# Optimization experiments

Hardware: AMD Instinct MI355X
Metric: run time of the kernel (lower is better)

Reference implementation:

```python
import jax, jax.numpy as jnp
import numpy as np

N_HEADS = 2
WINDOW = 4
BLOCK = 256


def _get_rel_emb(emb, length):
    # emb: [1, 2*WINDOW+1, K] -> [1, 2*length-1, K]
    pad = max(length - (WINDOW + 1), 0)
    start = max((WINDOW + 1) - length, 0)
    e = jnp.pad(emb, ((0, 0), (pad, pad), (0, 0)))
    return e[:, start:start + 2 * length - 1]


def _rel_to_abs(x):
    # x: [b, h, l, 2l-1] -> [b, h, l, l] (skew trick)
    b, h, l, _ = x.shape
    x = jnp.pad(x, ((0, 0), (0, 0), (0, 0), (0, 1))).reshape(b, h, 2 * l * l)
    x = jnp.pad(x, ((0, 0), (0, 0), (0, l - 1))).reshape(b, h, l + 1, 2 * l - 1)
    return x[:, :, :l, l - 1:]


def _abs_to_rel(x):
    # x: [b, h, l, l] -> [b, h, l, 2l-1] (inverse skew)
    b, h, l, _ = x.shape
    x = jnp.pad(x, ((0, 0), (0, 0), (0, 0), (0, l - 1))).reshape(b, h, l * (2 * l - 1))
    x = jnp.pad(x, ((0, 0), (0, 0), (l, 0))).reshape(b, h, l, 2 * l)
    return x[:, :, :, 1:]


def _attention(x, c, attn_mask, Wq, bq, Wk, bk, Wv, bv, Wo, bo, emb_rel_k, emb_rel_v):
    B, C, T = x.shape
    H, K = N_HEADS, C // N_HEADS
    # projections (torch Linear on [B,T,C])
    q = (jnp.einsum('bct,cd->btd', x, Wq) + bq).reshape(B, T, H, K).transpose(0, 2, 1, 3)
    k = (jnp.einsum('bct,cd->btd', c, Wk) + bk).reshape(B, T, H, K).transpose(0, 2, 1, 3)
    v = (jnp.einsum('bct,cd->btd', c, Wv) + bv).reshape(B, T, H, K).transpose(0, 2, 1, 3)
    qs = q / jnp.sqrt(jnp.float32(K))
    scores = jnp.einsum('bhtk,bhsk->bhts', qs, k)  # [B,H,T,T]
    # relative-position key logits (heads_share=True -> single table)
    rel_k = _get_rel_emb(emb_rel_k, T)[0]          # [2T-1, K]
    rel_logits = jnp.einsum('bhtk,rk->bhtr', qs, rel_k)
    scores = scores + _rel_to_abs(rel_logits)
    # proximal bias: -log1p(|i-j|)
    r = jnp.arange(T, dtype=jnp.float32)
    scores = scores - jnp.log1p(jnp.abs(r[:, None] - r[None, :]))[None, None]
    # attn mask + block-local mask (block mask active because mask is given)
    ij = jnp.arange(T)
    block_ok = jnp.abs(ij[:, None] - ij[None, :]) <= BLOCK
    valid = (attn_mask != 0) & block_ok[None, None]
    scores = jnp.where(valid, scores, jnp.float32(-1e4))
    p = jax.nn.softmax(scores, axis=-1)
    out = jnp.einsum('bhts,bhsk->bhtk', p, v)
    # relative-position value contribution
    rel_v = _get_rel_emb(emb_rel_v, T)[0]          # [2T-1, K]
    out = out + jnp.einsum('bhtr,rk->bhtk', _abs_to_rel(p), rel_v)
    out = out.transpose(0, 2, 1, 3).reshape(B, T, C)
    y = jnp.einsum('btd,do->bto', out, Wo) + bo
    return y.transpose(0, 2, 1)  # [B, out_channels, T]


def setup_inputs() -> dict:
    key = jax.random.key(0)
    ks = jax.random.split(key, 8)
    B, C, T = 4, 192, 2048
    K = C // N_HEADS
    s = jnp.float32(0.05)
    rel_std = jnp.float32(K ** -0.5)
    return {
        'x': jax.random.normal(ks[0], (B, C, T), jnp.float32),
        'c': jax.random.normal(ks[1], (B, C, T), jnp.float32),
        'Wq': jax.random.normal(ks[2], (C, C), jnp.float32) * s,
        'bq': jnp.zeros((C,), jnp.float32),
        'Wk': jax.random.normal(ks[3], (C, C), jnp.float32) * s,
        'bk': jnp.zeros((C,), jnp.float32),
        'Wv': jax.random.normal(ks[4], (C, C), jnp.float32) * s,
        'bv': jnp.zeros((C,), jnp.float32),
        'Wo': jax.random.normal(ks[5], (C, C), jnp.float32) * s,
        'bo': jnp.zeros((C,), jnp.float32),
        'emb_rel_k': jax.random.normal(ks[6], (1, 2 * WINDOW + 1, K), jnp.float32) * rel_std,
        'emb_rel_v': jax.random.normal(ks[7], (1, 2 * WINDOW + 1, K), jnp.float32) * rel_std,
        'attn_mask': jnp.ones((B, 1, T, T), jnp.int32),
    }


def reference(x, c, Wq, bq, Wk, bk, Wv, bv, Wo, bo, emb_rel_k, emb_rel_v, attn_mask):
    return _attention(x, c, attn_mask, Wq, bq, Wk, bk, Wv, bv, Wo, bo, emb_rel_k, emb_rel_v)
```

## Files before the change

kernel.cpp:

```cpp
#include <hip/hip_runtime.h>
#include <hip/hip_bf16.h>

#define B_DIM 4
#define C_DIM 192
#define T_SEQ 2048
#define H_DIM 2
#define K_DIM 96
#define BAND 256
#define IT 16
#define WSLOT 544
#define W_P 548
#define PMW 17

typedef __attribute__((ext_vector_type(8))) short bf16x8;
typedef __attribute__((ext_vector_type(4))) short bf16x4;
typedef __attribute__((ext_vector_type(4))) float f32x4;
#define MFMA16 __builtin_amdgcn_mfma_f32_16x16x32_bf16

__device__ __forceinline__ float bfbits2f(short s) {
    union { short s; __hip_bfloat16 h; } u; u.s = s; return __bfloat162float(u.h);
}
__device__ __forceinline__ short f2bf_bits(float f) {
    union { __hip_bfloat16 h; short s; } u; u.h = __float2bfloat16(f); return u.s;
}

#define OFF_WT(m)  ((size_t)(m)*73728)
#define OFF_BQS    ((size_t)294912)
#define OFF_RELKBF ((size_t)295680)
#define OFF_LT     ((size_t)298752)
#define OFF_PM     ((size_t)299840)
#define OFF_QBF    ((size_t)856896)
#define OFF_KBF    (OFF_QBF + 3145728)
#define OFF_VTB    (OFF_KBF + 3145728)
#define OFF_OBTC   (OFF_VTB + 3145728)

__global__ __launch_bounds__(256)
void prep_kernel(const float* __restrict__ Wq, const float* __restrict__ Wk,
                 const float* __restrict__ Wv, const float* __restrict__ Wo,
                 const float* __restrict__ bq, const float* __restrict__ relk,
                 const int* __restrict__ mask, char* __restrict__ ws)
{
    const float qscale = 0.10206207261596577f;
    const int bidx = blockIdx.x;
    const int tid  = threadIdx.x;

    if (bidx < 576) {
        const size_t idx = (size_t)bidx*256 + tid;
        const int mi  = (int)(idx / 36864);
        const int rem = (int)(idx % 36864);
        const int c = rem / C_DIM, d = rem % C_DIM;
        const float* src = (mi == 0) ? Wq : (mi == 1) ? Wk : (mi == 2) ? Wv : Wo;
        float v = src[c*C_DIM + d];
        if (mi == 0) v *= qscale;
        ((short*)(ws + OFF_WT(mi)))[d*C_DIM + c] = f2bf_bits(v);
        return;
    }
    if (bidx < 1120) {
        const int idx = (bidx - 576)*256 + tid;
        const int b = idx / (T_SEQ*PMW);
        const int rem = idx % (T_SEQ*PMW);
        const int i = rem / PMW, w = rem % PMW;
        const int jlo = max(0, (i & ~15) - BAND);
        const int* mrow = mask + ((size_t)b*T_SEQ + i)*T_SEQ;
        unsigned bits = 0;
        #pragma unroll
        for (int g4 = 0; g4 < 8; ++g4) {
            const int jg = jlo + 32*w + 4*g4;
            if (jg + 3 < T_SEQ) {
                const int4 mv = *reinterpret_cast<const int4*>(mrow + jg);
                bits |= (unsigned)(mv.x != 0) << (4*g4);
                bits |= (unsigned)(mv.y != 0) << (4*g4+1);
                bits |= (unsigned)(mv.z != 0) << (4*g4+2);
                bits |= (unsigned)(mv.w != 0) << (4*g4+3);
            } else {
                #pragma unroll
                for (int e = 0; e < 4; ++e)
                    if (jg + e < T_SEQ && mrow[jg+e] != 0) bits |= 1u << (4*g4+e);
            }
        }
        ((unsigned*)(ws + OFF_PM))[idx] = bits;
        return;
    }
    if (tid < C_DIM)
        ((float*)(ws + OFF_BQS))[tid] = bq[tid]*qscale;
    short* rkb = (short*)(ws + OFF_RELKBF);
    for (int idx = tid; idx < 16*K_DIM; idx += 256) {
        const int row = idx / K_DIM;
        rkb[idx] = (row < 9) ? f2bf_bits(relk[idx]) : (short)0;
    }
    float* ltws = (float*)(ws + OFF_LT);
    for (int idx = tid; idx < 257; idx += 256) ltws[idx] = log1pf((float)idx);
}

__global__ __launch_bounds__(256)
void proj_kernel(const float* __restrict__ x, const float* __restrict__ cin,
                 const float* __restrict__ bk, const float* __restrict__ bv,
                 char* __restrict__ ws)
{
    __shared__ short xs[IT*C_DIM];
    __shared__ short cs[IT*C_DIM];
    const int b    = blockIdx.x >> 8;
    const int half = (blockIdx.x >> 7) & 1;
    const int t0   = (blockIdx.x & 127) * IT;
    const int tid  = threadIdx.x;
    const int wave = tid >> 6, lane = tid & 63;
    const int q4 = lane >> 4, lr = lane & 15;

    for (int l = tid; l < 768; l += 256) {
        const int cr = l >> 2, u = l & 3;
        const size_t off = (size_t)(b*C_DIM + cr)*T_SEQ + t0 + 4*u;
        const float4 xv = *reinterpret_cast<const float4*>(x + off);
        const float4 cv = *reinterpret_cast<const float4*>(cin + off);
        xs[(4*u+0)*C_DIM + cr] = f2bf_bits(xv.x);
        xs[(4*u+1)*C_DIM + cr] = f2bf_bits(xv.y);
        xs[(4*u+2)*C_DIM + cr] = f2bf_bits(xv.z);
        xs[(4*u+3)*C_DIM + cr] = f2bf_bits(xv.w);
        cs[(4*u+0)*C_DIM + cr] = f2bf_bits(cv.x);
        cs[(4*u+1)*C_DIM + cr] = f2bf_bits(cv.y);
        cs[(4*u+2)*C_DIM + cr] = f2bf_bits(cv.z);
        cs[(4*u+3)*C_DIM + cr] = f2bf_bits(cv.w);
    }
    __syncthreads();

    const short* WqT = (const short*)(ws + OFF_WT(0));
    const short* WkT = (const short*)(ws + OFF_WT(1));
    const short* WvT = (const short*)(ws + OFF_WT(2));
    const float* bqs = (const float*)(ws + OFF_BQS);
    short* qbf = (short*)(ws + OFF_QBF);
    short* kbf = (short*)(ws + OFF_KBF);
    short* vtb = (short*)(ws + OFF_VTB);

    #pragma unroll
    for (int u = 0; u < 2; ++u) {
        if (u == 1 && wave >= 2) break;
        const int tl = (u == 0) ? wave : wave + 4;
        const int dt = half*6 + tl;
        f32x4 qa = {0,0,0,0}, ka = {0,0,0,0}, va = {0,0,0,0};
        #pragma unroll
        for (int kc = 0; kc < 6; ++kc) {
            const int ko = kc*32 + q4*8;
            const bf16x8 xf = *reinterpret_cast<const bf16x8*>(xs + lr*C_DIM + ko);
            const bf16x8 cf = *reinterpret_cast<const bf16x8*>(cs + lr*C_DIM + ko);
            const bf16x8 wqf = *reinterpret_cast<const bf16x8*>(WqT + (dt*16 + lr)*C_DIM + ko);
            const bf16x8 wkf = *reinterpret_cast<const bf16x8*>(WkT + (dt*16 + lr)*C_DIM + ko);
            const bf16x8 wvf = *reinterpret_cast<const bf16x8*>(WvT + (dt*16 + lr)*C_DIM + ko);
            qa = MFMA16(xf, wqf, qa, 0, 0, 0);
            ka = MFMA16(cf, wkf, ka, 0, 0, 0);
            va = MFMA16(wvf, cf, va, 0, 0, 0);
        }
        {
            const int d = dt*16 + lr, h = d/K_DIM, kk = d%K_DIM;
            const int bh = b*H_DIM + h;
            const float bq_v = bqs[d], bk_v = bk[d];
            #pragma unroll
            for (int e = 0; e < 4; ++e) {
                const int t = t0 + q4*4 + e;
                const size_t off = ((size_t)bh*T_SEQ + t)*K_DIM + kk;
                qbf[off] = f2bf_bits(qa[e] + bq_v);
                kbf[off] = f2bf_bits(ka[e] + bk_v);
            }
        }
        {
            #pragma unroll
            for (int e = 0; e < 4; ++e) {
                const int d = dt*16 + q4*4 + e, h = d/K_DIM, kk = d%K_DIM;
                const int bh = b*H_DIM + h;
                vtb[((size_t)bh*K_DIM + kk)*T_SEQ + t0 + lr] = f2bf_bits(va[e] + bv[d]);
            }
        }
    }
}

__global__ __launch_bounds__(256)
void attn_kernel(const float* __restrict__ relv, char* __restrict__ ws)
{
    __shared__ float p_s[IT*W_P];
    __shared__ float shbuf[864];
    __shared__ unsigned pml[IT*PMW];

    const short* qbf = (const short*)(ws + OFF_QBF);
    const short* kbf = (const short*)(ws + OFF_KBF);
    const short* vtb = (const short*)(ws + OFF_VTB);
    const short* rkb = (const short*)(ws + OFF_RELKBF);
    const float* ltws = (const float*)(ws + OFF_LT);
    const unsigned* pm = (const unsigned*)(ws + OFF_PM);
    short* obtc = (short*)(ws + OFF_OBTC);

    const int bh  = blockIdx.x >> 7;
    const int i0  = (blockIdx.x & 127) * IT;
    const int b   = bh / H_DIM;
    const int h   = bh % H_DIM;
    const int tid = threadIdx.x;
    const int wave = tid >> 6, lane = tid & 63;
    const int q4 = lane >> 4, lr = lane & 15;

    const int jlo  = max(0, i0 - BAND);
    const int jhi  = min(T_SEQ - 1, i0 + IT - 1 + BAND);
    const int wlen = jhi - jlo + 1;
    const size_t qkv_base = (size_t)bh * T_SEQ * K_DIM;

    float* lt = shbuf;
    float* rl = shbuf + 260;
    for (int idx = tid; idx < 257; idx += 256) lt[idx] = ltws[idx];
    for (int idx = tid; idx < IT*PMW; idx += 256)
        pml[idx] = pm[(b*T_SEQ + i0)*PMW + idx];

    bf16x8 qa[3];
    {
        const short* qrow = qbf + qkv_base + (size_t)(i0 + lr)*K_DIM + q4*8;
        #pragma unroll
        for (int kc = 0; kc < 3; ++kc)
            qa[kc] = *reinterpret_cast<const bf16x8*>(qrow + kc*32);
    }

    {
        int jt = wave;
        const short* kr0;
        {
            int jr = jlo + jt*16 + lr;
            if (jr > T_SEQ-1) jr = T_SEQ-1;
            kr0 = kbf + qkv_base + (size_t)jr*K_DIM + q4*8;
        }
        bf16x8 kb0 = *reinterpret_cast<const bf16x8*>(kr0);
        bf16x8 kb1 = *reinterpret_cast<const bf16x8*>(kr0 + 32);
        bf16x8 kb2 = *reinterpret_cast<const bf16x8*>(kr0 + 64);
        while (jt < WSLOT/16) {
            const int jtn = jt + 4;
            bf16x8 n0, n1, n2;
            if (jtn < WSLOT/16) {
                int jr = jlo + jtn*16 + lr;
                if (jr > T_SEQ-1) jr = T_SEQ-1;
                const short* krn = kbf + qkv_base + (size_t)jr*K_DIM + q4*8;
                n0 = *reinterpret_cast<const bf16x8*>(krn);
                n1 = *reinterpret_cast<const bf16x8*>(krn + 32);
                n2 = *reinterpret_cast<const bf16x8*>(krn + 64);
            }
            f32x4 s = {0.f,0.f,0.f,0.f};
            s = MFMA16(qa[0], kb0, s, 0, 0, 0);
            s = MFMA16(qa[1], kb1, s, 0, 0, 0);
            s = MFMA16(qa[2], kb2, s, 0, 0, 0);
            #pragma unroll
            for (int e = 0; e < 4; ++e)
                p_s[(q4*4 + e)*W_P + jt*16 + lr] = s[e];
            kb0 = n0; kb1 = n1; kb2 = n2;
            jt = jtn;
        }
    }
    if (wave == 3) {
        const short* krow = rkb + lr*K_DIM + q4*8;
        f32x4 s = {0.f,0.f,0.f,0.f};
        #pragma unroll
        for (int kc = 0; kc < 3; ++kc)
            s = MFMA16(qa[kc], *reinterpret_cast<const bf16x8*>(krow + kc*32), s, 0, 0, 0);
        if (lr < 9) {
            #pragma unroll
            for (int e = 0; e < 4; ++e)
                rl[(q4*4 + e)*9 + lr] = s[e];
        }
    }
    __syncthreads();

    {
        const int r = tid >> 4, sj = tid & 15;
        const int i = i0 + r;
        float vals[36];
        float m = -INFINITY;
        #pragma unroll
        for (int mm = 0; mm < 9; ++mm) {
            const int j0 = 4*sj + 64*mm;
            float4 pv = make_float4(0.f,0.f,0.f,0.f);
            unsigned mb = 0;
            if (j0 < WSLOT) {
                pv = *reinterpret_cast<const float4*>(p_s + r*W_P + j0);
                mb = pml[r*PMW + (j0 >> 5)] >> (j0 & 31);
            }
            const float pe[4] = {pv.x, pv.y, pv.z, pv.w};
            #pragma unroll
            for (int e = 0; e < 4; ++e) {
                const int j = j0 + e;
                float val = -INFINITY;
                if (j0 < WSLOT && j < wlen) {
                    const int jg = jlo + j, dd = jg - i;
                    const int ad = dd < 0 ? -dd : dd;
                    if (ad <= BAND && ((mb >> e) & 1)) {
                        val = pe[e] - lt[ad];
                        if ((unsigned)(dd + 4) <= 8u) val += rl[r*9 + dd + 4];
                    }
                }
                vals[mm*4 + e] = val;
                m = fmaxf(m, val);
            }
        }
        #pragma unroll
        for (int off = 8; off > 0; off >>= 1) m = fmaxf(m, __shfl_xor(m, off, 64));
        if (m == -INFINITY) m = 0.f;
        float ssum = 0.f;
        #pragma unroll
        for (int u = 0; u < 36; ++u) { vals[u] = __expf(vals[u] - m); ssum += vals[u]; }
        #pragma unroll
        for (int off = 8; off > 0; off >>= 1) ssum += __shfl_xor(ssum, off, 64);
        const float inv = ssum > 0.f ? 1.f/ssum : 0.f;
        short* pb = (short*)p_s;
        #pragma unroll
        for (int mm = 0; mm < 9; ++mm) {
            const int j0 = 4*sj + 64*mm;
            if (j0 < WSLOT) {
                bf16x4 w;
                #pragma unroll
                for (int e = 0; e < 4; ++e) w[e] = f2bf_bits(vals[mm*4+e]*inv);
                *reinterpret_cast<bf16x4*>(pb + r*(2*W_P) + j0) = w;
            }
        }
    }
    __syncthreads();

    for (int idx = tid; idx < 9*K_DIM; idx += 256) shbuf[idx] = relv[idx];

    const short* pb = (const short*)p_s;
    f32x4 o0 = {0.f,0.f,0.f,0.f}, o1 = {0.f,0.f,0.f,0.f};
    {
        auto vaddr = [&](int kcv)->const short* {
            int tc = jlo + kcv*32 + q4*8;
            if (tc > T_SEQ-8) tc = T_SEQ-8;
            return vtb + qkv_base + (size_t)lr*T_SEQ + tc;
        };
        const short* va0 = vaddr(0);
        bf16x8 vb0 = *reinterpret_cast<const bf16x8*>(va0 + (size_t)(wave*16)*T_SEQ);
        bf16x8 vb1;
        if (wave < 2) vb1 = *reinterpret_cast<const bf16x8*>(va0 + (size_t)((wave+4)*16)*T_SEQ);
        for (int kc = 0; kc < WSLOT/32; ++kc) {
            bf16x8 n0, n1;
            if (kc + 1 < WSLOT/32) {
                const short* van = vaddr(kc + 1);
                n0 = *reinterpret_cast<const bf16x8*>(van + (size_t)(wave*16)*T_SEQ);
                if (wave < 2) n1 = *reinterpret_cast<const bf16x8*>(van + (size_t)((wave+4)*16)*T_SEQ);
            }
            const bf16x8 pa = *reinterpret_cast<const bf16x8*>(pb + lr*(2*W_P) + kc*32 + q4*8);
            o0 = MFMA16(pa, vb0, o0, 0, 0, 0);
            if (wave < 2) o1 = MFMA16(pa, vb1, o1, 0, 0, 0);
            vb0 = n0; vb1 = n1;
        }
    }
    __syncthreads();

    #pragma unroll
    for (int u = 0; u < 2; ++u) {
        if (u == 1 && wave >= 2) break;
        const int nt = (u == 0) ? wave : wave + 4;
        const f32x4 oc = (u == 0) ? o0 : o1;
        const int col = nt*16 + lr;
        #pragma unroll
        for (int e = 0; e < 4; ++e) {
            const int row = q4*4 + e;
            const int i = i0 + row;
            float v = oc[e];
            #pragma unroll
            for (int dd = 0; dd < 9; ++dd) {
                const int jg = i + dd - 4;
                if (jg >= 0 && jg < T_SEQ)
                    v += bfbits2f(pb[row*(2*W_P) + (jg - jlo)]) * shbuf[dd*K_DIM + col];
            }
            obtc[((size_t)b*T_SEQ + i)*C_DIM + h*K_DIM + col] = f2bf_bits(v);
        }
    }
}

__global__ __launch_bounds__(256)
void oproj_kernel(const float* __restrict__ bo, float* __restrict__ y,
                  const char* __restrict__ ws)
{
    const int b    = blockIdx.x >> 8;
    const int half = (blockIdx.x >> 7) & 1;
    const int t0   = (blockIdx.x & 127) * 16;
    const int tid  = threadIdx.x;
    const int wave = tid >> 6, lane = tid & 63;
    const int q4 = lane >> 4, lr = lane & 15;

    const short* WoT  = (const short*)(ws + OFF_WT(3));
    const short* obtc = (const short*)(ws + OFF_OBTC);

    #pragma unroll
    for (int u = 0; u < 2; ++u) {
        if (u == 1 && wave >= 2) break;
        const int tl = (u == 0) ? wave : wave + 4;
        const int dt = half*6 + tl;
        f32x4 a = {0.f,0.f,0.f,0.f};
        #pragma unroll
        for (int kc = 0; kc < 6; ++kc) {
            const int ko = kc*32 + q4*8;
            const bf16x8 bf = *reinterpret_cast<const bf16x8*>(
                obtc + ((size_t)b*T_SEQ + t0 + lr)*C_DIM + ko);
            const bf16x8 af = *reinterpret_cast<const bf16x8*>(
                WoT + (dt*16 + lr)*C_DIM + ko);
            a = MFMA16(af, bf, a, 0, 0, 0);
        }
        #pragma unroll
        for (int e = 0; e < 4; ++e) {
            const int d = dt*16 + q4*4 + e;
            y[((size_t)b*C_DIM + d)*T_SEQ + t0 + lr] = a[e] + bo[d];
        }
    }
}

extern "C" void kernel_launch(void* const* d_in, const int* in_sizes, int n_in,
                              void* d_out, int out_size, void* d_ws, size_t ws_size,
                              hipStream_t stream)
{
    const float* x    = (const float*)d_in[0];
    const float* c    = (const float*)d_in[1];
    const float* Wq   = (const float*)d_in[2];
    const float* bq   = (const float*)d_in[3];
    const float* Wk   = (const float*)d_in[4];
    const float* bk   = (const float*)d_in[5];
    const float* Wv   = (const float*)d_in[6];
    const float* bv   = (const float*)d_in[7];
    const float* Wo   = (const float*)d_in[8];
    const float* bo   = (const float*)d_in[9];
    const float* relk = (const float*)d_in[10];
    const float* relv = (const float*)d_in[11];
    const int*   mask = (const int*)d_in[12];
    float*       y    = (float*)d_out;
    char*        ws   = (char*)d_ws;

    hipLaunchKernelGGL(prep_kernel, dim3(1121), dim3(256), 0, stream,
                       Wq, Wk, Wv, Wo, bq, relk, mask, ws);
    hipLaunchKernelGGL(proj_kernel, dim3(B_DIM*2*(T_SEQ/16)), dim3(256), 0, stream,
                       x, c, bk, bv, ws);
    hipLaunchKernelGGL(attn_kernel, dim3(B_DIM*H_DIM*(T_SEQ/IT)), dim3(256), 0, stream,
                       relv, ws);
    hipLaunchKernelGGL(oproj_kernel, dim3(B_DIM*2*(T_SEQ/16)), dim3(256), 0, stream,
                       bo, y, ws);
}
```

Baseline: 181.6 us.

## Fuse mask bit-packing into attention kernel and simplify K/V load loops

Moves the attention-mask bit-packing out of the prep kernel and into the attention kernel, so each block packs its own 16 rows straight from the int mask. This removes the packed-mask workspace round trip and shrinks the prep grid. The prep weight transpose now reads float4 vectors. The manual register double-buffering of K and V loads in the attention loops is replaced with plain loads, relying on the compiler and occupancy to hide latency. The risk is slower attention blocks from the extra mask reads and the lost software prefetch.

```diff
diff --git a/kernel.cpp b/kernel.cpp
--- a/kernel.cpp
+++ b/kernel.cpp
@@ -28,8 +28,7 @@
 #define OFF_BQS    ((size_t)294912)
 #define OFF_RELKBF ((size_t)295680)
 #define OFF_LT     ((size_t)298752)
-#define OFF_PM     ((size_t)299840)
-#define OFF_QBF    ((size_t)856896)
+#define OFF_QBF    ((size_t)299840)
 #define OFF_KBF    (OFF_QBF + 3145728)
 #define OFF_VTB    (OFF_KBF + 3145728)
 #define OFF_OBTC   (OFF_VTB + 3145728)
@@ -38,47 +37,25 @@
 void prep_kernel(const float* __restrict__ Wq, const float* __restrict__ Wk,
                  const float* __restrict__ Wv, const float* __restrict__ Wo,
                  const float* __restrict__ bq, const float* __restrict__ relk,
-                 const int* __restrict__ mask, char* __restrict__ ws)
+                 char* __restrict__ ws)
 {
     const float qscale = 0.10206207261596577f;
     const int bidx = blockIdx.x;
     const int tid  = threadIdx.x;
 
-    if (bidx < 576) {
-        const size_t idx = (size_t)bidx*256 + tid;
-        const int mi  = (int)(idx / 36864);
-        const int rem = (int)(idx % 36864);
+    if (bidx < 144) {
+        const size_t idx4 = ((size_t)bidx*256 + tid)*4;
+        const int mi  = (int)(idx4 / 36864);
+        const int rem = (int)(idx4 % 36864);
         const int c = rem / C_DIM, d = rem % C_DIM;
         const float* src = (mi == 0) ? Wq : (mi == 1) ? Wk : (mi == 2) ? Wv : Wo;
-        float v = src[c*C_DIM + d];
-        if (mi == 0) v *= qscale;
-        ((short*)(ws + OFF_WT(mi)))[d*C_DIM + c] = f2bf_bits(v);
-        return;
-    }
-    if (bidx < 1120) {
-        const int idx = (bidx - 576)*256 + tid;
-        const int b = idx / (T_SEQ*PMW);
-        const int rem = idx % (T_SEQ*PMW);
-        const int i = rem / PMW, w = rem % PMW;
-        const int jlo = max(0, (i & ~15) - BAND);
-        const int* mrow = mask + ((size_t)b*T_SEQ + i)*T_SEQ;
-        unsigned bits = 0;
-        #pragma unroll
-        for (int g4 = 0; g4 < 8; ++g4) {
-            const int jg = jlo + 32*w + 4*g4;
-            if (jg + 3 < T_SEQ) {
-                const int4 mv = *reinterpret_cast<const int4*>(mrow + jg);
-                bits |= (unsigned)(mv.x != 0) << (4*g4);
-                bits |= (unsigned)(mv.y != 0) << (4*g4+1);
-                bits |= (unsigned)(mv.z != 0) << (4*g4+2);
-                bits |= (unsigned)(mv.w != 0) << (4*g4+3);
-            } else {
-                #pragma unroll
-                for (int e = 0; e < 4; ++e)
-                    if (jg + e < T_SEQ && mrow[jg+e] != 0) bits |= 1u << (4*g4+e);
-            }
-        }
-        ((unsigned*)(ws + OFF_PM))[idx] = bits;
+        float4 v = *reinterpret_cast<const float4*>(src + c*C_DIM + d);
+        if (mi == 0) { v.x *= qscale; v.y *= qscale; v.z *= qscale; v.w *= qscale; }
+        short* wt = (short*)(ws + OFF_WT(mi));
+        wt[(d+0)*C_DIM + c] = f2bf_bits(v.x);
+        wt[(d+1)*C_DIM + c] = f2bf_bits(v.y);
+        wt[(d+2)*C_DIM + c] = f2bf_bits(v.z);
+        wt[(d+3)*C_DIM + c] = f2bf_bits(v.w);
         return;
     }
     if (tid < C_DIM)
@@ -172,7 +149,8 @@
 }
 
 __global__ __launch_bounds__(256)
-void attn_kernel(const float* __restrict__ relv, char* __restrict__ ws)
+void attn_kernel(const float* __restrict__ relv, const int* __restrict__ mask,
+                 char* __restrict__ ws)
 {
     __shared__ float p_s[IT*W_P];
     __shared__ float shbuf[864];
@@ -183,7 +161,6 @@
     const short* vtb = (const short*)(ws + OFF_VTB);
     const short* rkb = (const short*)(ws + OFF_RELKBF);
     const float* ltws = (const float*)(ws + OFF_LT);
-    const unsigned* pm = (const unsigned*)(ws + OFF_PM);
     short* obtc = (short*)(ws + OFF_OBTC);
 
     const int bh  = blockIdx.x >> 7;
@@ -202,8 +179,28 @@
     float* lt = shbuf;
     float* rl = shbuf + 260;
     for (int idx = tid; idx < 257; idx += 256) lt[idx] = ltws[idx];
-    for (int idx = tid; idx < IT*PMW; idx += 256)
-        pml[idx] = pm[(b*T_SEQ + i0)*PMW + idx];
+
+    for (int idx = tid; idx < IT*PMW; idx += 256) {
+        const int r = idx / PMW, w = idx % PMW;
+        const int* mrow = mask + ((size_t)b*T_SEQ + i0 + r)*T_SEQ;
+        unsigned bits = 0;
+        #pragma unroll
+        for (int g4 = 0; g4 < 8; ++g4) {
+            const int jg = jlo + 32*w + 4*g4;
+            if (jg + 3 < T_SEQ) {
+                const int4 mv = *reinterpret_cast<const int4*>(mrow + jg);
+                bits |= (unsigned)(mv.x != 0) << (4*g4);
+                bits |= (unsigned)(mv.y != 0) << (4*g4+1);
+                bits |= (unsigned)(mv.z != 0) << (4*g4+2);
+                bits |= (unsigned)(mv.w != 0) << (4*g4+3);
+            } else {
+                #pragma unroll
+                for (int e = 0; e < 4; ++e)
+                    if (jg + e < T_SEQ && mrow[jg+e] != 0) bits |= 1u << (4*g4+e);
+            }
+        }
+        pml[idx] = bits;
+    }
 
     bf16x8 qa[3];
     {
@@ -213,38 +210,17 @@
             qa[kc] = *reinterpret_cast<const bf16x8*>(qrow + kc*32);
     }
 
-    {
-        int jt = wave;
-        const short* kr0;
-        {
-            int jr = jlo + jt*16 + lr;
-            if (jr > T_SEQ-1) jr = T_SEQ-1;
-            kr0 = kbf + qkv_base + (size_t)jr*K_DIM + q4*8;
-        }
-        bf16x8 kb0 = *reinterpret_cast<const bf16x8*>(kr0);
-        bf16x8 kb1 = *reinterpret_cast<const bf16x8*>(kr0 + 32);
-        bf16x8 kb2 = *reinterpret_cast<const bf16x8*>(kr0 + 64);
-        while (jt < WSLOT/16) {
-            const int jtn = jt + 4;
-            bf16x8 n0, n1, n2;
-            if (jtn < WSLOT/16) {
-                int jr = jlo + jtn*16 + lr;
-                if (jr > T_SEQ-1) jr = T_SEQ-1;
-                const short* krn = kbf + qkv_base + (size_t)jr*K_DIM + q4*8;
-                n0 = *reinterpret_cast<const bf16x8*>(krn);
-                n1 = *reinterpret_cast<const bf16x8*>(krn + 32);
-                n2 = *reinterpret_cast<const bf16x8*>(krn + 64);
-            }
-            f32x4 s = {0.f,0.f,0.f,0.f};
-            s = MFMA16(qa[0], kb0, s, 0, 0, 0);
-            s = MFMA16(qa[1], kb1, s, 0, 0, 0);
-            s = MFMA16(qa[2], kb2, s, 0, 0, 0);
-            #pragma unroll
-            for (int e = 0; e < 4; ++e)
-                p_s[(q4*4 + e)*W_P + jt*16 + lr] = s[e];
-            kb0 = n0; kb1 = n1; kb2 = n2;
-            jt = jtn;
-        }
+    for (int jt = wave; jt < WSLOT/16; jt += 4) {
+        int jr = jlo + jt*16 + lr;
+        if (jr > T_SEQ-1) jr = T_SEQ-1;
+        const short* krow = kbf + qkv_base + (size_t)jr*K_DIM + q4*8;
+        f32x4 s = {0.f,0.f,0.f,0.f};
+        #pragma unroll
+        for (int kc = 0; kc < 3; ++kc)
+            s = MFMA16(qa[kc], *reinterpret_cast<const bf16x8*>(krow + kc*32), s, 0, 0, 0);
+        #pragma unroll
+        for (int e = 0; e < 4; ++e)
+            p_s[(q4*4 + e)*W_P + jt*16 + lr] = s[e];
     }
     if (wave == 3) {
         const short* krow = rkb + lr*K_DIM + q4*8;
@@ -318,27 +294,17 @@
 
     const short* pb = (const short*)p_s;
     f32x4 o0 = {0.f,0.f,0.f,0.f}, o1 = {0.f,0.f,0.f,0.f};
-    {
-        auto vaddr = [&](int kcv)->const short* {
-            int tc = jlo + kcv*32 + q4*8;
-            if (tc > T_SEQ-8) tc = T_SEQ-8;
-            return vtb + qkv_base + (size_t)lr*T_SEQ + tc;
-        };
-        const short* va0 = vaddr(0);
-        bf16x8 vb0 = *reinterpret_cast<const bf16x8*>(va0 + (size_t)(wave*16)*T_SEQ);
-        bf16x8 vb1;
-        if (wave < 2) vb1 = *reinterpret_cast<const bf16x8*>(va0 + (size_t)((wave+4)*16)*T_SEQ);
-        for (int kc = 0; kc < WSLOT/32; ++kc) {
-            bf16x8 n0, n1;
-            if (kc + 1 < WSLOT/32) {
-                const short* van = vaddr(kc + 1);
-                n0 = *reinterpret_cast<const bf16x8*>(van + (size_t)(wave*16)*T_SEQ);
-                if (wave < 2) n1 = *reinterpret_cast<const bf16x8*>(van + (size_t)((wave+4)*16)*T_SEQ);
-            }
-            const bf16x8 pa = *reinterpret_cast<const bf16x8*>(pb + lr*(2*W_P) + kc*32 + q4*8);
-            o0 = MFMA16(pa, vb0, o0, 0, 0, 0);
-            if (wave < 2) o1 = MFMA16(pa, vb1, o1, 0, 0, 0);
-            vb0 = n0; vb1 = n1;
+    for (int kc = 0; kc < WSLOT/32; ++kc) {
+        const bf16x8 pa = *reinterpret_cast<const bf16x8*>(pb + lr*(2*W_P) + kc*32 + q4*8);
+        int tc = jlo + kc*32 + q4*8;
+        if (tc > T_SEQ-8) tc = T_SEQ-8;
+        const bf16x8 vb0 = *reinterpret_cast<const bf16x8*>(
+            vtb + qkv_base + (size_t)(wave*16 + lr)*T_SEQ + tc);
+        o0 = MFMA16(pa, vb0, o0, 0, 0, 0);
+        if (wave < 2) {
+            const bf16x8 vb1 = *reinterpret_cast<const bf16x8*>(
+                vtb + qkv_base + (size_t)((wave+4)*16 + lr)*T_SEQ + tc);
+            o1 = MFMA16(pa, vb1, o1, 0, 0, 0);
         }
     }
     __syncthreads();
@@ -422,12 +388,12 @@
     float*       y    = (float*)d_out;
     char*        ws   = (char*)d_ws;
 
-    hipLaunchKernelGGL(prep_kernel, dim3(1121), dim3(256), 0, stream,
-                       Wq, Wk, Wv, Wo, bq, relk, mask, ws);
+    hipLaunchKernelGGL(prep_kernel, dim3(145), dim3(256), 0, stream,
+                       Wq, Wk, Wv, Wo, bq, relk, ws);
     hipLaunchKernelGGL(proj_kernel, dim3(B_DIM*2*(T_SEQ/16)), dim3(256), 0, stream,
                        x, c, bk, bv, ws);
     hipLaunchKernelGGL(attn_kernel, dim3(B_DIM*H_DIM*(T_SEQ/IT)), dim3(256), 0, stream,
-                       relv, ws);
+                       relv, mask, ws);
     hipLaunchKernelGGL(oproj_kernel, dim3(B_DIM*2*(T_SEQ/16)), dim3(256), 0, stream,
                        bo, y, ws);
 }
```

After: 189.2 us. 1.04x slower.
